# Performance work log

Measured on AMD Instinct MI355X. Metric: run time of the kernel, lower is better.

The kernel has to match this reference:

```python
import jax, jax.numpy as jnp
import numpy as np

DIM = 768
HEADS = 12
HEAD_DIM = DIM // HEADS          # 64
M = int(DIM * 0.5)               # 384 random features
HIDDEN = int(DIM * 4.0)          # 3072
SCALE = HEAD_DIM ** (-0.25)
EPSILON = 1e-8
LN_EPS = 1e-5


def _orf(key):
    # per-head block-orthogonal random features, scaled by sqrt(m)
    def one(k):
        a = jax.random.normal(k, (M, HEAD_DIM))
        q, _ = jnp.linalg.qr(a)          # (M, HEAD_DIM), orthonormal columns
        return q.T                        # (HEAD_DIM, M), orthonormal rows
    ks = jax.random.split(key, HEADS)
    return jax.vmap(one)(ks) * np.sqrt(M)  # (H, HEAD_DIM, M)


def setup_inputs() -> dict:
    key = jax.random.key(0)
    ks = jax.random.split(key, 8)
    s = 0.02
    return {
        "x": jax.random.normal(ks[0], (32, 1024, DIM), jnp.float32),
        "ln1_g": jnp.ones((DIM,), jnp.float32),
        "ln1_b": jnp.zeros((DIM,), jnp.float32),
        "qkv_w": jax.random.normal(ks[1], (DIM, 3 * DIM), jnp.float32) * s,
        "qkv_b": jnp.zeros((3 * DIM,), jnp.float32),
        "w_orf": _orf(ks[2]).astype(jnp.float32),
        "proj_w": jax.random.normal(ks[3], (DIM, DIM), jnp.float32) * s,
        "proj_b": jnp.zeros((DIM,), jnp.float32),
        "ln2_g": jnp.ones((DIM,), jnp.float32),
        "ln2_b": jnp.zeros((DIM,), jnp.float32),
        "fc1_w": jax.random.normal(ks[4], (DIM, HIDDEN), jnp.float32) * s,
        "fc1_b": jnp.zeros((HIDDEN,), jnp.float32),
        "fc2_w": jax.random.normal(ks[5], (HIDDEN, DIM), jnp.float32) * s,
        "fc2_b": jnp.zeros((DIM,), jnp.float32),
    }


def _layernorm(x, g, b):
    mu = jnp.mean(x, axis=-1, keepdims=True)
    var = jnp.mean(jnp.square(x - mu), axis=-1, keepdims=True)
    return (x - mu) * jax.lax.rsqrt(var + LN_EPS) * g + b


def _feature_map(x, w):
    # x: (B,H,N,C), w: (H,C,M) -> exp(x*scale @ w - ||x*scale||^2/2)/sqrt(M)
    xs = x * SCALE
    proj = jnp.einsum("bhnc,hcm->bhnm", xs, w)
    sq = 0.5 * jnp.sum(xs * xs, axis=-1, keepdims=True)
    return jnp.exp(proj - sq) / np.sqrt(M)


def _performer_attn(x, qkv_w, qkv_b, w_orf, proj_w, proj_b):
    B, N, _ = x.shape
    qkv = x @ qkv_w + qkv_b                       # (B,N,3*DIM)
    qkv = qkv.reshape(B, N, 3, HEADS, HEAD_DIM)
    qkv = jnp.transpose(qkv, (2, 0, 3, 1, 4))     # (3,B,H,N,C)
    q = _feature_map(qkv[0], w_orf)               # (B,H,N,M)
    k = _feature_map(qkv[1], w_orf)               # (B,H,N,M)
    v = qkv[2]                                    # (B,H,N,C)
    k_sum = jnp.sum(k, axis=2)                    # (B,H,M)
    D = jnp.einsum("bhnm,bhm->bhn", q, k_sum)[..., None] + EPSILON
    ktv = jnp.einsum("bhnm,bhnc->bhmc", k, v)     # (B,H,M,C)
    out = jnp.einsum("bhnm,bhmc->bhnc", q, ktv) / D
    out = jnp.transpose(out, (0, 2, 1, 3)).reshape(B, N, DIM)
    return out @ proj_w + proj_b


def reference(x, ln1_g, ln1_b, qkv_w, qkv_b, w_orf, proj_w, proj_b,
              ln2_g, ln2_b, fc1_w, fc1_b, fc2_w, fc2_b):
    h = x + _performer_attn(_layernorm(x, ln1_g, ln1_b),
                            qkv_w, qkv_b, w_orf, proj_w, proj_b)
    y = _layernorm(h, ln2_g, ln2_b)
    y = jax.nn.gelu(y @ fc1_w + fc1_b) @ fc2_w + fc2_b
    return h + y
```

## Files before the change

### kernel.cpp

```cpp
#include <hip/hip_runtime.h>
#include <hip/hip_bf16.h>

#define NTOK   32768
#define BATCH  32
#define SEQ    1024
#define DIMD   768
#define HEADS  12
#define HDIM   64
#define MFEAT  384
#define HIDDEN 3072
#define SCALE  0.35355339059327379f
#define HALF_SCALE2 0.0625f
#define EPSP   3.84e-6f
#define WSCL   64.0f
#define IWSCL  0.015625f

typedef __attribute__((ext_vector_type(8))) short bf16x8;
typedef __attribute__((ext_vector_type(4))) float f32x4;

static __device__ __forceinline__ float bf2f(unsigned short u) {
    return __uint_as_float(((unsigned)u) << 16);
}
static __device__ __forceinline__ unsigned short f2bf(float f) {
    unsigned u = __float_as_uint(f);
    return (unsigned short)((u + 0x7FFFu + ((u >> 16) & 1u)) >> 16);
}
static __device__ __forceinline__ unsigned char f2e4m3(float f) {
    unsigned u = __float_as_uint(f);
    const unsigned char s = (unsigned char)((u >> 24) & 0x80);
    const float af = __uint_as_float(u & 0x7FFFFFFF);
    if (!(af < 464.0f)) return s | 0x7E;
    int e = (int)((u >> 23) & 0xFF) - 127;
    if (e < -6) e = -6;
    const float ulp = __uint_as_float((unsigned)((e - 3 + 127) << 23));
    const float q = rintf(af / ulp) * ulp;
    if (q == 0.0f) return s;
    const unsigned v = __float_as_uint(q);
    const int qe = (int)((v >> 23) & 0xFF) - 127;
    if (qe < -6) return s | (unsigned char)(q * 512.0f);
    return s | (unsigned char)(((qe + 7) << 3) | ((v >> 20) & 7));
}
static __device__ __forceinline__ unsigned char f2e4m3_hw(float v) {
    unsigned r = 0;
    asm("v_cvt_pk_fp8_f32 %0, %1, %1" : "+v"(r) : "v"(v));
    return (unsigned char)(r & 0xFF);
}
static __device__ __forceinline__ float gelu_fast(float v) {
    const float c = 0.7978845608028654f;
    const float u = c * v * (1.0f + 0.044715f * v * v);
    return v / (1.0f + __expf(-2.0f * u));
}
static __device__ __forceinline__ void gload16(const void* g, void* l) {
    __builtin_amdgcn_global_load_lds(
        (const __attribute__((address_space(1))) void*)g,
        (__attribute__((address_space(3))) void*)l, 16, 0, 0);
}

template <int OT>
__global__ __launch_bounds__(256) void ln_vec(
    const float* __restrict__ x, const float* __restrict__ g,
    const float* __restrict__ bta, void* __restrict__ o) {
    const size_t row = blockIdx.x;
    const float* xr = x + row * DIMD;
    const int t = threadIdx.x;
    float4 v = make_float4(0.f, 0.f, 0.f, 0.f);
    if (t < 192) v = *(const float4*)(xr + t * 4);
    float s  = v.x + v.y + v.z + v.w;
    float sq = v.x * v.x + v.y * v.y + v.z * v.z + v.w * v.w;
    const int lane = t & 63, w = t >> 6;
    #pragma unroll
    for (int off = 32; off > 0; off >>= 1) {
        s  += __shfl_down(s, off, 64);
        sq += __shfl_down(sq, off, 64);
    }
    __shared__ float red[2][4];
    if (lane == 0) { red[0][w] = s; red[1][w] = sq; }
    __syncthreads();
    s  = red[0][0] + red[0][1] + red[0][2] + red[0][3];
    sq = red[1][0] + red[1][1] + red[1][2] + red[1][3];
    const float mu  = s * (1.0f / DIMD);
    const float var = sq * (1.0f / DIMD) - mu * mu;
    const float r = rsqrtf(var + 1e-5f);
    if (t < 192) {
        const float4 gv = *(const float4*)(g + t * 4);
        const float4 bv = *(const float4*)(bta + t * 4);
        const float o0 = (v.x - mu) * r * gv.x + bv.x;
        const float o1 = (v.y - mu) * r * gv.y + bv.y;
        const float o2 = (v.z - mu) * r * gv.z + bv.z;
        const float o3 = (v.w - mu) * r * gv.w + bv.w;
        if constexpr (OT == 1) {
            unsigned short* orow = (unsigned short*)o + row * DIMD + t * 4;
            *(ushort4*)orow = make_ushort4(f2bf(o0), f2bf(o1), f2bf(o2), f2bf(o3));
        } else {
            unsigned char* orow = (unsigned char*)o + row * DIMD + t * 4;
            uchar4 p; p.x = f2e4m3(o0); p.y = f2e4m3(o1);
            p.z = f2e4m3(o2); p.w = f2e4m3(o3);
            *(uchar4*)orow = p;
        }
    }
}

__global__ __launch_bounds__(256) void wconv(
    const float* __restrict__ W, unsigned short* __restrict__ Wt, int K, int N) {
    __shared__ float tile[32][33];
    const int n0 = blockIdx.x << 5, k0 = blockIdx.y << 5;
    const int tn = threadIdx.x & 31, tg = threadIdx.x >> 5;
    #pragma unroll
    for (int i = 0; i < 4; ++i) {
        const int k = (tg << 2) + i;
        tile[k][tn] = W[(size_t)(k0 + k) * N + n0 + tn];
    }
    __syncthreads();
    #pragma unroll
    for (int i = 0; i < 4; ++i) {
        const int n = (tg << 2) + i;
        Wt[(size_t)(n0 + n) * K + k0 + tn] = f2bf(tile[tn][n]);
    }
}

__global__ __launch_bounds__(256) void wconv_f8(
    const float* __restrict__ W, unsigned char* __restrict__ Wt, int K, int N) {
    __shared__ float tile[32][33];
    const int n0 = blockIdx.x << 5, k0 = blockIdx.y << 5;
    const int tn = threadIdx.x & 31, tg = threadIdx.x >> 5;
    #pragma unroll
    for (int i = 0; i < 4; ++i) {
        const int k = (tg << 2) + i;
        tile[k][tn] = W[(size_t)(k0 + k) * N + n0 + tn];
    }
    __syncthreads();
    #pragma unroll
    for (int i = 0; i < 4; ++i) {
        const int n = (tg << 2) + i;
        Wt[(size_t)(n0 + n) * K + k0 + tn] = f2e4m3(WSCL * tile[tn][n]);
    }
}

__global__ __launch_bounds__(256) void wprep(
    const float* __restrict__ worf, unsigned short* __restrict__ worf_ts) {
    __shared__ float tile[32][33];
    const int m0 = blockIdx.x << 5, c0 = blockIdx.y << 5, h = blockIdx.z;
    const int tn = threadIdx.x & 31, tg = threadIdx.x >> 5;
    #pragma unroll
    for (int i = 0; i < 4; ++i) {
        const int c = (tg << 2) + i;
        tile[c][tn] = worf[(size_t)(h * HDIM + c0 + c) * MFEAT + m0 + tn];
    }
    __syncthreads();
    #pragma unroll
    for (int i = 0; i < 4; ++i) {
        const int m = (tg << 2) + i;
        worf_ts[(size_t)(h * MFEAT + m0 + m) * HDIM + c0 + tn] =
            f2bf(SCALE * tile[tn][m]);
    }
}

template <int ACT, bool RES, bool OBF16>
__global__ __launch_bounds__(256, 2) void gemm_mfma(
    const unsigned short* __restrict__ A, const unsigned short* __restrict__ Wt,
    const float* __restrict__ bias, const float* __restrict__ resid,
    void* __restrict__ Craw, int K, int N) {
    __shared__ unsigned short As[3][128 * 32];
    __shared__ unsigned short Bs[3][128 * 32];
    const int t = threadIdx.x;
    const int w = t >> 6, l = t & 63;
    const int ncol = gridDim.x;
    const int lin = blockIdx.y * ncol + blockIdx.x;
    const int cpx = (ncol * gridDim.y) >> 3;
    const int wg = (lin & 7) * cpx + (lin >> 3);
    const int row0 = (wg / ncol) << 7, col0 = (wg % ncol) << 7;
    const int wr = (w >> 1) << 6, wc = (w & 1) << 6;

    const int sc = (((l & 3) ^ ((l >> 3) & 3)) << 3);
    const unsigned short* ag0 = A  + (size_t)(row0 + w * 32 + (l >> 2)) * K + sc;
    const unsigned short* ag1 = ag0 + (size_t)16 * K;
    const unsigned short* bg0 = Wt + (size_t)(col0 + w * 32 + (l >> 2)) * K + sc;
    const unsigned short* bg1 = bg0 + (size_t)16 * K;

    f32x4 acc[4][4] = {};
    const int NT = K >> 5;

    auto stage = [&](int bi, int s) {
        const size_t ko = (size_t)s << 5;
        gload16(ag0 + ko, &As[bi][w * 1024]);
        gload16(ag1 + ko, &As[bi][w * 1024 + 512]);
        gload16(bg0 + ko, &Bs[bi][w * 1024]);
        gload16(bg1 + ko, &Bs[bi][w * 1024 + 512]);
    };

    stage(0, 0);
    stage(1, 1);
    const int lr = l & 15, lg = l >> 4;
    const int lkx = (lg << 3) ^ ((((lr >> 1) & 3)) << 3);
    int cur = 0;
    for (int s = 0; s < NT; ++s) {
        if (s + 1 < NT) asm volatile("s_waitcnt vmcnt(4)" ::: "memory");
        else            asm volatile("s_waitcnt vmcnt(0)" ::: "memory");
        __builtin_amdgcn_s_barrier();
        __builtin_amdgcn_sched_barrier(0);
        if (s + 2 < NT) {
            int sb = cur + 2; if (sb >= 3) sb -= 3;
            stage(sb, s + 2);
        }
        const unsigned short* ab = &As[cur][0];
        const unsigned short* bb = &Bs[cur][0];
        bf16x8 af[4], bfr[4];
        #pragma unroll
        for (int f = 0; f < 4; ++f) {
            af[f]  = *(const bf16x8*)(ab + (wr + f * 16 + lr) * 32 + lkx);
            bfr[f] = *(const bf16x8*)(bb + (wc + f * 16 + lr) * 32 + lkx);
        }
        #pragma unroll
        for (int fi = 0; fi < 4; ++fi)
            #pragma unroll
            for (int fj = 0; fj < 4; ++fj)
                acc[fi][fj] = __builtin_amdgcn_mfma_f32_16x16x32_bf16(
                    af[fi], bfr[fj], acc[fi][fj], 0, 0, 0);
        cur = (cur + 1 == 3) ? 0 : cur + 1;
    }

    float bv[4];
    #pragma unroll
    for (int fj = 0; fj < 4; ++fj) bv[fj] = bias[col0 + wc + fj * 16 + lr];
    #pragma unroll
    for (int fi = 0; fi < 4; ++fi) {
        #pragma unroll
        for (int r = 0; r < 4; ++r) {
            const int row = row0 + wr + fi * 16 + lg * 4 + r;
            const size_t base = (size_t)row * N + col0 + wc + lr;
            #pragma unroll
            for (int fj = 0; fj < 4; ++fj) {
                float v = acc[fi][fj][r] + bv[fj];
                if constexpr (RES) v += resid[base + fj * 16];
                if constexpr (ACT == 1) v = gelu_fast(v);
                if constexpr (OBF16) ((unsigned short*)Craw)[base + fj * 16] = f2bf(v);
                else                 ((float*)Craw)[base + fj * 16] = v;
            }
        }
    }
}

template <int ACT, bool RES, int OT>
__global__ __launch_bounds__(256, 2) void gemm_fp8(
    const unsigned char* __restrict__ A, const unsigned char* __restrict__ Wt,
    const float* __restrict__ bias, const float* __restrict__ resid,
    void* __restrict__ Craw, int K, int N) {
    __shared__ unsigned char As[3][8192];
    __shared__ unsigned char Bs[3][8192];
    const int t = threadIdx.x;
    const int w = t >> 6, l = t & 63;
    const int ncol = gridDim.x;
    const int lin = blockIdx.y * ncol + blockIdx.x;
    const int cpx = (ncol * gridDim.y) >> 3;
    const int wg = (lin & 7) * cpx + (lin >> 3);
    const int row0 = (wg / ncol) << 7, col0 = (wg % ncol) << 7;
    const int wr = (w >> 1) << 6, wc = (w & 1) << 6;

    const int sch = (((l & 3) ^ ((l >> 3) & 3)) << 4);
    const unsigned char* ag[2];
    const unsigned char* bg[2];
    #pragma unroll
    for (int j = 0; j < 2; ++j) {
        const int r = j * 64 + w * 16 + (l >> 2);
        ag[j] = A  + (size_t)(row0 + r) * K + sch;
        bg[j] = Wt + (size_t)(col0 + r) * K + sch;
    }

    f32x4 acc[4][4] = {};
    const int NT = K >> 6;

    auto stage = [&](int bi, int s) {
        const size_t ko = (size_t)s << 6;
        #pragma unroll
        for (int j = 0; j < 2; ++j) {
            gload16(ag[j] + ko, &As[bi][j * 4096 + w * 1024]);
            gload16(bg[j] + ko, &Bs[bi][j * 4096 + w * 1024]);
        }
    };

    stage(0, 0);
    stage(1, 1);
    const int lr = l & 15, lg = l >> 4;
    const int m2 = (lr >> 1) & 3;
    const int xo0 = ((((lg >> 1) ^ m2) << 4) | ((lg & 1) << 3));
    const int xo1 = xo0 ^ 32;
    int cur = 0;
    for (int s = 0; s < NT; ++s) {
        if (s + 1 < NT) asm volatile("s_waitcnt vmcnt(4)" ::: "memory");
        else            asm volatile("s_waitcnt vmcnt(0)" ::: "memory");
        __builtin_amdgcn_s_barrier();
        __builtin_amdgcn_sched_barrier(0);
        if (s + 2 < NT) {
            int sb = cur + 2; if (sb >= 3) sb -= 3;
            stage(sb, s + 2);
        }
        const unsigned char* ab = &As[cur][0];
        const unsigned char* bb = &Bs[cur][0];
        long long av[4][2], bvv[4][2];
        #pragma unroll
        for (int f = 0; f < 4; ++f) {
            const int ra = (wr + f * 16 + lr) << 6;
            const int rb = (wc + f * 16 + lr) << 6;
            av[f][0]  = *(const long long*)(ab + ra + xo0);
            av[f][1]  = *(const long long*)(ab + ra + xo1);
            bvv[f][0] = *(const long long*)(bb + rb + xo0);
            bvv[f][1] = *(const long long*)(bb + rb + xo1);
        }
        #pragma unroll
        for (int ks = 0; ks < 2; ++ks)
            #pragma unroll
            for (int fi = 0; fi < 4; ++fi)
                #pragma unroll
                for (int fj = 0; fj < 4; ++fj)
                    acc[fi][fj] = __builtin_amdgcn_mfma_f32_16x16x32_fp8_fp8(
                        av[fi][ks], bvv[fj][ks], acc[fi][fj], 0, 0, 0);
        cur = (cur + 1 == 3) ? 0 : cur + 1;
    }

    float bv[4];
    #pragma unroll
    for (int fj = 0; fj < 4; ++fj) bv[fj] = bias[col0 + wc + fj * 16 + lr];
    #pragma unroll
    for (int fi = 0; fi < 4; ++fi) {
        #pragma unroll
        for (int r = 0; r < 4; ++r) {
            const int row = row0 + wr + fi * 16 + lg * 4 + r;
            const size_t base = (size_t)row * N + col0 + wc + lr;
            #pragma unroll
            for (int fj = 0; fj < 4; ++fj) {
                float v = acc[fi][fj][r] * IWSCL + bv[fj];
                if constexpr (RES) v += resid[base + fj * 16];
                if constexpr (ACT == 1) v = gelu_fast(v);
                if constexpr (OT == 2) ((unsigned char*)Craw)[base + fj * 16] = f2e4m3_hw(v);
                else                   ((float*)Craw)[base + fj * 16] = v;
            }
        }
    }
}

__global__ __launch_bounds__(256, 1) void ktv_mfma(
    const unsigned short* __restrict__ qkvb,
    const unsigned short* __restrict__ worf_ts,
    unsigned short* __restrict__ ktvT) {
    const int h = blockIdx.x, b = blockIdx.y, bh = b * HEADS + h;
    __shared__ __align__(16) unsigned short Klds[32][72];
    __shared__ __align__(16) unsigned short VT[80][40];
    __shared__ __align__(16) unsigned short P[4][96][40];
    const int t = threadIdx.x, w = t >> 6, l = t & 63;
    const int lr = l & 15, lg = l >> 4;
    const int m0 = w * 96;

    bf16x8 bfw[6][2];
    #pragma unroll
    for (int mt = 0; mt < 6; ++mt)
        #pragma unroll
        for (int ks = 0; ks < 2; ++ks)
            bfw[mt][ks] = *(const bf16x8*)(worf_ts +
                (size_t)(h * MFEAT + m0 + mt * 16 + lr) * HDIM + ks * 32 + lg * 8);

    f32x4 acc[5][6] = {};

    for (int i = t; i < 16 * 40; i += 256) {
        const int r = 64 + i / 40, cc = i % 40;
        VT[r][cc] = (r == 64) ? (unsigned short)0x3F80 : (unsigned short)0;
    }
    const unsigned short* kglob = qkvb + (size_t)b * SEQ * 2304 + 768 + h * 64;
    const unsigned short* vglob = kglob + 768;

    for (int n0 = 0; n0 < SEQ; n0 += 32) {
        __syncthreads();
        {
            const int row = t >> 3, c8 = (t & 7) << 3;
            *(bf16x8*)&Klds[row][c8] =
                *(const bf16x8*)(kglob + (size_t)(n0 + row) * 2304 + c8);
        }
        {
            const int n = t & 31, c0 = (t >> 5) << 3;
            const unsigned short* src = vglob + (size_t)(n0 + n) * 2304 + c0;
            ushort4 v0 = *(const ushort4*)src;
            ushort4 v1 = *(const ushort4*)(src + 4);
            VT[c0 + 0][n] = v0.x; VT[c0 + 1][n] = v0.y;
            VT[c0 + 2][n] = v0.z; VT[c0 + 3][n] = v0.w;
            VT[c0 + 4][n] = v1.x; VT[c0 + 5][n] = v1.y;
            VT[c0 + 6][n] = v1.z; VT[c0 + 7][n] = v1.w;
        }
        __syncthreads();

        bf16x8 afk[2][2];
        float sqv[2][4];
        #pragma unroll
        for (int ns = 0; ns < 2; ++ns) {
            float s = 0.f;
            #pragma unroll
            for (int ks = 0; ks < 2; ++ks) {
                afk[ns][ks] = *(const bf16x8*)&Klds[ns * 16 + lr][ks * 32 + lg * 8];
                #pragma unroll
                for (int j = 0; j < 8; ++j) {
                    const float f = bf2f((unsigned short)afk[ns][ks][j]);
                    s += f * f;
                }
            }
            s += __shfl_xor(s, 16);
            s += __shfl_xor(s, 32);
            s *= HALF_SCALE2;
            #pragma unroll
            for (int r = 0; r < 4; ++r)
                sqv[ns][r] = __shfl(s, (lg << 2) + r);
        }

        #pragma unroll
        for (int mt = 0; mt < 6; ++mt) {
            #pragma unroll
            for (int ns = 0; ns < 2; ++ns) {
                f32x4 p = {};
                p = __builtin_amdgcn_mfma_f32_16x16x32_bf16(afk[ns][0], bfw[mt][0], p, 0, 0, 0);
                p = __builtin_amdgcn_mfma_f32_16x16x32_bf16(afk[ns][1], bfw[mt][1], p, 0, 0, 0);
                ushort4 pk;
                pk.x = f2bf(__expf(p[0] - sqv[ns][0]));
                pk.y = f2bf(__expf(p[1] - sqv[ns][1]));
                pk.z = f2bf(__expf(p[2] - sqv[ns][2]));
                pk.w = f2bf(__expf(p[3] - sqv[ns][3]));
                *(ushort4*)&P[w][mt * 16 + lr][ns * 16 + lg * 4] = pk;
            }
        }
        asm volatile("s_waitcnt lgkmcnt(0)" ::: "memory");
        __builtin_amdgcn_sched_barrier(0);

        bf16x8 afv[5];
        #pragma unroll
        for (int ct = 0; ct < 5; ++ct)
            afv[ct] = *(const bf16x8*)&VT[ct * 16 + lr][lg * 8];
        #pragma unroll
        for (int mt = 0; mt < 6; ++mt) {
            const bf16x8 bp = *(const bf16x8*)&P[w][mt * 16 + lr][lg * 8];
            #pragma unroll
            for (int ct = 0; ct < 5; ++ct)
                acc[ct][mt] = __builtin_amdgcn_mfma_f32_16x16x32_bf16(afv[ct], bp, acc[ct][mt], 0, 0, 0);
        }
    }

    unsigned short* dst = ktvT + (size_t)bh * 80 * MFEAT;
    #pragma unroll
    for (int ct = 0; ct < 5; ++ct)
        #pragma unroll
        for (int mt = 0; mt < 6; ++mt)
            #pragma unroll
            for (int r = 0; r < 4; ++r) {
                const int cc = ct * 16 + lg * 4 + r;
                const int m = m0 + mt * 16 + lr;
                dst[(size_t)cc * MFEAT + m] = f2bf(acc[ct][mt][r]);
            }
}

__global__ __launch_bounds__(256) void attn_out_mfma(
    const unsigned short* __restrict__ qkvb,
    const unsigned short* __restrict__ worf_ts,
    const unsigned short* __restrict__ ktvT,
    unsigned short* __restrict__ attn) {
    const int n0 = blockIdx.x << 7;
    const int h = blockIdx.y, b = blockIdx.z, bh = b * HEADS + h;
    __shared__ __align__(16) unsigned short KT[80][104];
    __shared__ __align__(16) unsigned short P[4][32][104];
    const int t = threadIdx.x, w = t >> 6, l = t & 63;
    const int lr = l & 15, lg = l >> 4;
    const int nw = n0 + w * 32;

    bf16x8 bq[2][2];
    float sqn[2];
    #pragma unroll
    for (int nt = 0; nt < 2; ++nt) {
        float s = 0.f;
        #pragma unroll
        for (int ks = 0; ks < 2; ++ks) {
            bq[nt][ks] = *(const bf16x8*)(qkvb +
                (size_t)(b * SEQ + nw + nt * 16 + lr) * 2304 + h * 64 + ks * 32 + lg * 8);
            #pragma unroll
            for (int j = 0; j < 8; ++j) {
                const float f = bf2f((unsigned short)bq[nt][ks][j]);
                s += f * f;
            }
        }
        s += __shfl_xor(s, 16);
        s += __shfl_xor(s, 32);
        sqn[nt] = s * HALF_SCALE2;
    }

    f32x4 acc[5][2] = {};
    const unsigned short* ktg = ktvT + (size_t)bh * 80 * MFEAT;

    for (int ch = 0; ch < 4; ++ch) {
        const int m0 = ch * 96;
        __syncthreads();
        for (int i = t; i < 1920; i += 256) {
            const int row = i / 24, q = i % 24;
            *(ushort4*)&KT[row][q * 4] =
                *(const ushort4*)(ktg + (size_t)row * MFEAT + m0 + q * 4);
        }
        __syncthreads();

        #pragma unroll
        for (int mt = 0; mt < 6; ++mt) {
            bf16x8 afw[2];
            #pragma unroll
            for (int ks = 0; ks < 2; ++ks)
                afw[ks] = *(const bf16x8*)(worf_ts +
                    (size_t)(h * MFEAT + m0 + mt * 16 + lr) * HDIM + ks * 32 + lg * 8);
            #pragma unroll
            for (int nt = 0; nt < 2; ++nt) {
                f32x4 p = {};
                p = __builtin_amdgcn_mfma_f32_16x16x32_bf16(afw[0], bq[nt][0], p, 0, 0, 0);
                p = __builtin_amdgcn_mfma_f32_16x16x32_bf16(afw[1], bq[nt][1], p, 0, 0, 0);
                ushort4 pk;
                pk.x = f2bf(__expf(p[0] - sqn[nt]));
                pk.y = f2bf(__expf(p[1] - sqn[nt]));
                pk.z = f2bf(__expf(p[2] - sqn[nt]));
                pk.w = f2bf(__expf(p[3] - sqn[nt]));
                *(ushort4*)&P[w][nt * 16 + lr][mt * 16 + lg * 4] = pk;
            }
        }
        asm volatile("s_waitcnt lgkmcnt(0)" ::: "memory");
        __builtin_amdgcn_sched_barrier(0);

        #pragma unroll
        for (int ks = 0; ks < 3; ++ks) {
            bf16x8 bp[2];
            #pragma unroll
            for (int nt = 0; nt < 2; ++nt)
                bp[nt] = *(const bf16x8*)&P[w][nt * 16 + lr][ks * 32 + lg * 8];
            #pragma unroll
            for (int ct = 0; ct < 5; ++ct) {
                const bf16x8 av = *(const bf16x8*)&KT[ct * 16 + lr][ks * 32 + lg * 8];
                #pragma unroll
                for (int nt = 0; nt < 2; ++nt)
                    acc[ct][nt] = __builtin_amdgcn_mfma_f32_16x16x32_bf16(av, bp[nt], acc[ct][nt], 0, 0, 0);
            }
        }
    }

    #pragma unroll
    for (int nt = 0; nt < 2; ++nt) {
        const float d = __shfl(acc[4][nt][0], lr);
        const float inv = 1.0f / (d + EPSP);
        const int token = b * SEQ + nw + nt * 16 + lr;
        #pragma unroll
        for (int ct = 0; ct < 4; ++ct)
            #pragma unroll
            for (int r = 0; r < 4; ++r) {
                const int cc = ct * 16 + lg * 4 + r;
                attn[(size_t)token * DIMD + h * 64 + cc] = f2bf(acc[ct][nt][r] * inv);
            }
    }
}

extern "C" void kernel_launch(void* const* d_in, const int* in_sizes, int n_in,
                              void* d_out, int out_size, void* d_ws, size_t ws_size,
                              hipStream_t stream) {
    const float* x      = (const float*)d_in[0];
    const float* ln1_g  = (const float*)d_in[1];
    const float* ln1_b  = (const float*)d_in[2];
    const float* qkv_w  = (const float*)d_in[3];
    const float* qkv_b  = (const float*)d_in[4];
    const float* w_orf  = (const float*)d_in[5];
    const float* proj_w = (const float*)d_in[6];
    const float* proj_b = (const float*)d_in[7];
    const float* ln2_g  = (const float*)d_in[8];
    const float* ln2_b  = (const float*)d_in[9];
    const float* fc1_w  = (const float*)d_in[10];
    const float* fc1_b  = (const float*)d_in[11];
    const float* fc2_w  = (const float*)d_in[12];
    const float* fc2_b  = (const float*)d_in[13];
    float* out = (float*)d_out;

    char* wsb = (char*)d_ws;
    unsigned short* qkvb    = (unsigned short*)wsb;
    unsigned short* attn    = (unsigned short*)(wsb + 150994944);
    unsigned short* ktvT    = (unsigned short*)(wsb + 201326592);
    unsigned short* worf_ts = (unsigned short*)(wsb + 224919552);
    unsigned char*  y2f8    = (unsigned char*)(wsb + 201326592);
    unsigned char*  hidf8   = (unsigned char*)wsb;
    unsigned short* qkv_wt  = (unsigned short*)(wsb + 251658240);
    unsigned short* proj_wt = (unsigned short*)(wsb + 255197184);
    unsigned char*  fc1_wf8 = (unsigned char*)(wsb + 256376832);
    unsigned char*  fc2_wf8 = (unsigned char*)(wsb + 261095424);
    unsigned short* xln     = (unsigned short*)d_out;

    wconv<<<dim3(2304 / 32, 768 / 32), 256, 0, stream>>>(qkv_w, qkv_wt, DIMD, 2304);
    wconv<<<dim3(768 / 32, 768 / 32), 256, 0, stream>>>(proj_w, proj_wt, DIMD, DIMD);
    wconv_f8<<<dim3(3072 / 32, 768 / 32), 256, 0, stream>>>(fc1_w, fc1_wf8, DIMD, HIDDEN);
    wconv_f8<<<dim3(768 / 32, 3072 / 32), 256, 0, stream>>>(fc2_w, fc2_wf8, HIDDEN, DIMD);
    wprep<<<dim3(MFEAT / 32, HDIM / 32, HEADS), 256, 0, stream>>>(w_orf, worf_ts);
    ln_vec<1><<<NTOK, 256, 0, stream>>>(x, ln1_g, ln1_b, xln);
    gemm_mfma<0, false, true><<<dim3(2304 / 128, NTOK / 128), 256, 0, stream>>>(
        xln, qkv_wt, qkv_b, nullptr, qkvb, DIMD, 2304);
    ktv_mfma<<<dim3(HEADS, BATCH), 256, 0, stream>>>(qkvb, worf_ts, ktvT);
    attn_out_mfma<<<dim3(SEQ / 128, HEADS, BATCH), 256, 0, stream>>>(
        qkvb, worf_ts, ktvT, attn);
    gemm_mfma<0, true, false><<<dim3(DIMD / 128, NTOK / 128), 256, 0, stream>>>(
        attn, proj_wt, proj_b, x, out, DIMD, DIMD);
    ln_vec<2><<<NTOK, 256, 0, stream>>>(out, ln2_g, ln2_b, y2f8);
    gemm_fp8<1, false, 2><<<dim3(HIDDEN / 128, NTOK / 128), 256, 0, stream>>>(
        y2f8, fc1_wf8, fc1_b, nullptr, hidf8, DIMD, HIDDEN);
    gemm_fp8<0, true, 0><<<dim3(DIMD / 128, NTOK / 128), 256, 0, stream>>>(
        hidf8, fc2_wf8, fc2_b, out, out, HIDDEN, DIMD);
}
```

Before: 802.9 us.

## Permute FP8 K layout so each lane reads 16 contiguous bytes from LDS

Stores FP8 activations and weights in a permuted K order within each 64-element block. Each lane's two 8-byte MFMA operands for the two k-steps then sit next to each other, so one 16-byte LDS read replaces two 8-byte reads. The layernorm, weight-conversion and FP8-output GEMM epilogue writers all apply the same permutation, and the global-to-LDS staging row mapping is simplified. The risks are byte-scattered epilogue stores and every producer and consumer needing to agree on the permutation.

```diff
diff --git a/kernel.cpp b/kernel.cpp
--- a/kernel.cpp
+++ b/kernel.cpp
@@ -17,6 +17,7 @@
 
 typedef __attribute__((ext_vector_type(8))) short bf16x8;
 typedef __attribute__((ext_vector_type(4))) float f32x4;
+typedef __attribute__((ext_vector_type(2))) long long llong2;
 
 static __device__ __forceinline__ float bf2f(unsigned short u) {
     return __uint_as_float(((unsigned)u) << 16);
@@ -44,6 +45,9 @@
     unsigned r = 0;
     asm("v_cvt_pk_fp8_f32 %0, %1, %1" : "+v"(r) : "v"(v));
     return (unsigned char)(r & 0xFF);
+}
+static __device__ __forceinline__ int kperm(int kl) {
+    return ((kl & 31) >> 3) * 16 + ((kl >> 5) << 3) + (kl & 7);
 }
 static __device__ __forceinline__ float gelu_fast(float v) {
     const float c = 0.7978845608028654f;
@@ -92,7 +96,9 @@
             unsigned short* orow = (unsigned short*)o + row * DIMD + t * 4;
             *(ushort4*)orow = make_ushort4(f2bf(o0), f2bf(o1), f2bf(o2), f2bf(o3));
         } else {
-            unsigned char* orow = (unsigned char*)o + row * DIMD + t * 4;
+            const int k = t * 4;
+            const int kb = k & ~63, kl = k & 63;
+            unsigned char* orow = (unsigned char*)o + row * DIMD + kb + kperm(kl);
             uchar4 p; p.x = f2e4m3(o0); p.y = f2e4m3(o1);
             p.z = f2e4m3(o2); p.w = f2e4m3(o3);
             *(uchar4*)orow = p;
@@ -132,7 +138,9 @@
     #pragma unroll
     for (int i = 0; i < 4; ++i) {
         const int n = (tg << 2) + i;
-        Wt[(size_t)(n0 + n) * K + k0 + tn] = f2e4m3(WSCL * tile[tn][n]);
+        const int k = k0 + tn;
+        const int kb = k & ~63, kl = k & 63;
+        Wt[(size_t)(n0 + n) * K + kb + kperm(kl)] = f2e4m3(WSCL * tile[tn][n]);
     }
 }
 
@@ -256,34 +264,27 @@
     const int row0 = (wg / ncol) << 7, col0 = (wg % ncol) << 7;
     const int wr = (w >> 1) << 6, wc = (w & 1) << 6;
 
-    const int sch = (((l & 3) ^ ((l >> 3) & 3)) << 4);
-    const unsigned char* ag[2];
-    const unsigned char* bg[2];
-    #pragma unroll
-    for (int j = 0; j < 2; ++j) {
-        const int r = j * 64 + w * 16 + (l >> 2);
-        ag[j] = A  + (size_t)(row0 + r) * K + sch;
-        bg[j] = Wt + (size_t)(col0 + r) * K + sch;
-    }
+    const int sc = (((l & 3) ^ ((l >> 3) & 3)) << 4);
+    const unsigned char* ag0 = A  + (size_t)(row0 + w * 32 + (l >> 2)) * K + sc;
+    const unsigned char* ag1 = ag0 + (size_t)16 * K;
+    const unsigned char* bg0 = Wt + (size_t)(col0 + w * 32 + (l >> 2)) * K + sc;
+    const unsigned char* bg1 = bg0 + (size_t)16 * K;
 
     f32x4 acc[4][4] = {};
     const int NT = K >> 6;
 
     auto stage = [&](int bi, int s) {
         const size_t ko = (size_t)s << 6;
-        #pragma unroll
-        for (int j = 0; j < 2; ++j) {
-            gload16(ag[j] + ko, &As[bi][j * 4096 + w * 1024]);
-            gload16(bg[j] + ko, &Bs[bi][j * 4096 + w * 1024]);
-        }
+        gload16(ag0 + ko, &As[bi][w * 2048]);
+        gload16(ag1 + ko, &As[bi][w * 2048 + 1024]);
+        gload16(bg0 + ko, &Bs[bi][w * 2048]);
+        gload16(bg1 + ko, &Bs[bi][w * 2048 + 1024]);
     };
 
     stage(0, 0);
     stage(1, 1);
     const int lr = l & 15, lg = l >> 4;
-    const int m2 = (lr >> 1) & 3;
-    const int xo0 = ((((lg >> 1) ^ m2) << 4) | ((lg & 1) << 3));
-    const int xo1 = xo0 ^ 32;
+    const int xoff = ((lg ^ ((lr >> 1) & 3)) << 4);
     int cur = 0;
     for (int s = 0; s < NT; ++s) {
         if (s + 1 < NT) asm volatile("s_waitcnt vmcnt(4)" ::: "memory");
@@ -296,15 +297,11 @@
         }
         const unsigned char* ab = &As[cur][0];
         const unsigned char* bb = &Bs[cur][0];
-        long long av[4][2], bvv[4][2];
+        llong2 av[4], bvv[4];
         #pragma unroll
         for (int f = 0; f < 4; ++f) {
-            const int ra = (wr + f * 16 + lr) << 6;
-            const int rb = (wc + f * 16 + lr) << 6;
-            av[f][0]  = *(const long long*)(ab + ra + xo0);
-            av[f][1]  = *(const long long*)(ab + ra + xo1);
-            bvv[f][0] = *(const long long*)(bb + rb + xo0);
-            bvv[f][1] = *(const long long*)(bb + rb + xo1);
+            av[f]  = *(const llong2*)(ab + ((wr + f * 16 + lr) << 6) + xoff);
+            bvv[f] = *(const llong2*)(bb + ((wc + f * 16 + lr) << 6) + xoff);
         }
         #pragma unroll
         for (int ks = 0; ks < 2; ++ks)
@@ -331,8 +328,13 @@
                 float v = acc[fi][fj][r] * IWSCL + bv[fj];
                 if constexpr (RES) v += resid[base + fj * 16];
                 if constexpr (ACT == 1) v = gelu_fast(v);
-                if constexpr (OT == 2) ((unsigned char*)Craw)[base + fj * 16] = f2e4m3_hw(v);
-                else                   ((float*)Craw)[base + fj * 16] = v;
+                if constexpr (OT == 2) {
+                    const int cl = (fj << 4) + lr;
+                    ((unsigned char*)Craw)[(size_t)row * N + col0 + wc + kperm(cl)] =
+                        f2e4m3_hw(v);
+                } else {
+                    ((float*)Craw)[base + fj * 16] = v;
+                }
             }
         }
     }
```

Result: no change. 793.4 us (-1.2%).
